# Optimization experiments

Hardware: AMD Instinct MI355X
Metric: run time of the kernel (lower is better)

The kernel has to match this reference:

```python
import jax, jax.numpy as jnp
import numpy as np
from functools import partial

NUM_CLUSTERS = 64
KMEANS_ITERS = 10  # fixed Lloyd iterations standing in for sklearn's converged fit


def _assign(points, centers):
    # points: [M, D], centers: [K, D] -> labels [M]
    # squared L2 distance via expansion; the -|x|^2 term is constant per point
    d = jnp.sum(centers * centers, axis=1)[None, :] - 2.0 * (points @ centers.T)
    return jnp.argmin(d, axis=1)


def _kmeans_fit_predict(points, num_clusters, iters):
    # Deterministic init: first K points (fixed-seed sklearn stand-in).
    centers0 = points[:num_clusters]

    def step(centers, _):
        labels = _assign(points, centers)
        sums = jax.ops.segment_sum(points, labels, num_segments=num_clusters)
        counts = jax.ops.segment_sum(jnp.ones((points.shape[0],), points.dtype),
                                     labels, num_segments=num_clusters)
        new_centers = jnp.where(counts[:, None] > 0, sums / jnp.maximum(counts, 1.0)[:, None], centers)
        return new_centers, None

    centers, _ = jax.lax.scan(step, centers0, None, length=iters)
    labels = _assign(points, centers)
    return labels, centers


def setup_inputs() -> dict:
    key = jax.random.key(0)
    k1, k2, k3 = jax.random.split(key, 3)
    B, N, D = 16, 4096, 384
    x = jax.random.normal(k1, (B, N, D), dtype=jnp.float32)
    # nn.Linear(feature_dim, feature_dim): weight [out, in], bias [out]
    scale = 1.0 / np.sqrt(D)
    W = jax.random.uniform(k2, (D, D), dtype=jnp.float32, minval=-scale, maxval=scale)
    b = jax.random.uniform(k3, (D,), dtype=jnp.float32, minval=-scale, maxval=scale)
    return {"x": x, "W": W, "b": b}


def reference(x, W, b):
    B, N, D = x.shape
    x_flat = jax.lax.stop_gradient(x.reshape(-1, D))  # torch does .detach() before kmeans
    labels, centers = _kmeans_fit_predict(x_flat, NUM_CLUSTERS, KMEANS_ITERS)
    clustered = centers[labels].reshape(B, N, D)
    return clustered @ W.T + b
```

## Files before the change

kernel.cpp:

```cpp
#include <hip/hip_runtime.h>

#define P_TOT 65536
#define DIM   384
#define KCL   64
#define ITERS 10
#define BPTS  256
#define NSB   8
#define BK    32
#define NKT   (DIM / BK)
#define LKA   36
#define LKB   68


__global__ __launch_bounds__(384) void init_kernel(const float* __restrict__ x,
                                                   float* __restrict__ centers,
                                                   float* __restrict__ cnorm,
                                                   float* __restrict__ cnt,
                                                   float* __restrict__ sums) {
    __shared__ float red[384];
    const int c = blockIdx.x, t = threadIdx.x;
    float v = x[(size_t)c * DIM + t];
    centers[(size_t)c * DIM + t] = v;
#pragma unroll
    for (int b = 0; b < NSB; ++b) sums[(size_t)b * KCL * DIM + (size_t)c * DIM + t] = 0.f;
    if (t == 0) cnt[c] = 0.f;
    red[t] = v * v;
    __syncthreads();
    if (t < 128) red[t] = red[t] + red[t + 128] + red[t + 256];
    __syncthreads();
    for (int s = 64; s > 0; s >>= 1) {
        if (t < s) red[t] += red[t + s];
        __syncthreads();
    }
    if (t == 0) cnorm[c] = red[0];
}

#define GEMM_ARGMIN_BODY(X, CENTERS, CNORM)                                          \
    const int t   = threadIdx.x;                                                     \
    const int cg  = t & 15;                               \
    const int pg  = t >> 4;                          \
    const int p0  = blockIdx.x * BPTS;                                               \
    const int spt = t >> 1;                             \
    const int sah = (t & 1) * 16;                      \
    const int sbc = t >> 3;                            \
    const int sbk = (t & 7) * 4;                \
    if (t < KCL) scn[t] = (CNORM)[t];                                                \
    float acc[8][4];                                                                 \
    _Pragma("unroll")                                                                \
    for (int i = 0; i < 8; ++i)                                                      \
        _Pragma("unroll")                                                            \
        for (int j = 0; j < 4; ++j) acc[i][j] = 0.f;                                 \
    const float* xrow = (X) + (size_t)(p0 + spt) * DIM;                              \
    const float* crow = (CENTERS) + (size_t)sbc * DIM;                               \
    float4 ra0 = *(const float4*)(xrow + sah);                                       \
    float4 ra1 = *(const float4*)(xrow + sah + 4);                                   \
    float4 ra2 = *(const float4*)(xrow + sah + 8);                                   \
    float4 ra3 = *(const float4*)(xrow + sah + 12);                                  \
    float4 rb  = *(const float4*)(crow + sbk);                                       \
    for (int kt = 0; kt < NKT; ++kt) {                                               \
        const int cur = kt & 1;                                                      \
        *(float4*)&At[cur][spt][sah + 0]  = ra0;                                     \
        *(float4*)&At[cur][spt][sah + 4]  = ra1;                                     \
        *(float4*)&At[cur][spt][sah + 8]  = ra2;                                     \
        *(float4*)&At[cur][spt][sah + 12] = ra3;                                     \
        Bt[cur][sbk + 0][sbc] = rb.x;  Bt[cur][sbk + 1][sbc] = rb.y;                 \
        Bt[cur][sbk + 2][sbc] = rb.z;  Bt[cur][sbk + 3][sbc] = rb.w;                 \
        if (kt + 1 < NKT) {                        \
            const int k0 = (kt + 1) * BK;                                            \
            ra0 = *(const float4*)(xrow + k0 + sah);                                 \
            ra1 = *(const float4*)(xrow + k0 + sah + 4);                             \
            ra2 = *(const float4*)(xrow + k0 + sah + 8);                             \
            ra3 = *(const float4*)(xrow + k0 + sah + 12);                            \
            rb  = *(const float4*)(crow + k0 + sbk);                                 \
        }                                                                            \
        __syncthreads();                  \
        _Pragma("unroll")                                                            \
        for (int kq = 0; kq < 8; ++kq) {                                             \
            float af[8][4];                                                          \
            _Pragma("unroll")                                                        \
            for (int i = 0; i < 8; ++i) {                                            \
                const float4 a4 = *(const float4*)&At[cur][pg * 8 + i][kq * 4];      \
                af[i][0] = a4.x; af[i][1] = a4.y; af[i][2] = a4.z; af[i][3] = a4.w;  \
            }                                                                        \
            _Pragma("unroll")                                                        \
            for (int kk = 0; kk < 4; ++kk) {                                         \
                const float4 bf = *(const float4*)&Bt[cur][kq * 4 + kk][cg * 4];     \
                _Pragma("unroll")                                                    \
                for (int i = 0; i < 8; ++i) {                                        \
                    acc[i][0] += af[i][kk] * bf.x;                                   \
                    acc[i][1] += af[i][kk] * bf.y;                                   \
                    acc[i][2] += af[i][kk] * bf.z;                                   \
                    acc[i][3] += af[i][kk] * bf.w;                                   \
                }                                                                    \
            }                                                                        \
        }                                                                            \
    }                                                                                \
    {                                                                                \
        float cn[4];                                                                 \
        _Pragma("unroll")                                                            \
        for (int j = 0; j < 4; ++j) cn[j] = scn[cg * 4 + j];                         \
        _Pragma("unroll")                                                            \
        for (int i = 0; i < 8; ++i) {                                                \
            float bvv = 3.4e38f; int bc = 0;                                         \
            _Pragma("unroll")                                                        \
            for (int j = 0; j < 4; ++j) {                                            \
                float d = cn[j] - 2.0f * acc[i][j];                                  \
                if (d < bvv) { bvv = d; bc = cg * 4 + j; }      \
            }                                                                        \
            _Pragma("unroll")                                                        \
            for (int m = 1; m < 16; m <<= 1) {       \
                const float ov = __shfl_xor(bvv, m, 64);                             \
                const int   oc = __shfl_xor(bc, m, 64);                              \
                if (ov < bvv || (ov == bvv && oc < bc)) { bvv = ov; bc = oc; }       \
            }                                                                        \
            if ((t & 15) == 0) lab[pg * 8 + i] = bc;                                 \
        }                                                                            \
    }                                                                                \
    __syncthreads();

__global__ __launch_bounds__(512, 2) void fused_kernel(const float* __restrict__ x,
                                                       const float* __restrict__ centers,
                                                       const float* __restrict__ cnorm,
                                                       float* __restrict__ sums,
                                                       float* __restrict__ cnt) {
    __shared__ float At[2][BPTS][LKA];
    __shared__ float Bt[2][BK][LKB];
    __shared__ float scn[KCL];
    __shared__ int   lab[BPTS];
    __shared__ int   lcnt[KCL];
    __shared__ int   lstart[KCL + 1];
    __shared__ int   lcur[KCL];
    __shared__ int   order[BPTS];

    if (threadIdx.x < KCL) lcnt[threadIdx.x] = 0;

    GEMM_ARGMIN_BODY(x, centers, cnorm)

    int myl = -1;
    if (t < BPTS) {
        myl = lab[t];
        atomicAdd(&lcnt[myl], 1);
    }
    __syncthreads();
    if (t < 64) {
        int v = lcnt[t];
        int s = v;
#pragma unroll
        for (int d = 1; d < 64; d <<= 1) {
            int u = __shfl_up(s, d, 64);
            if (t >= d) s += u;
        }
        lstart[t] = s - v;
        lcur[t] = s - v;
        if (t == 63) lstart[64] = s;
    }
    __syncthreads();
    if (t < BPTS) {
        int pos = atomicAdd(&lcur[myl], 1);
        order[pos] = t;
    }
    __syncthreads();

    if (t < DIM) {
        const float* xb = x + (size_t)p0 * DIM;
        float* sb = sums + (size_t)(blockIdx.x & (NSB - 1)) * KCL * DIM;
        int   curc = lab[order[0]];
        float run  = 0.f;
        for (int j0 = 0; j0 < BPTS; j0 += 8) {
            float v[8]; int cc[8];
#pragma unroll
            for (int u = 0; u < 8; ++u) {
                const int p = order[j0 + u];
                cc[u] = lab[p];
                v[u]  = xb[(size_t)p * DIM + t];
            }
#pragma unroll
            for (int u = 0; u < 8; ++u) {
                if (cc[u] != curc) {
                    atomicAdd(&sb[curc * DIM + t], run);
                    run = 0.f; curc = cc[u];
                }
                run += v[u];
            }
        }
        atomicAdd(&sb[curc * DIM + t], run);
    }
    if (t < KCL && lcnt[t] > 0) atomicAdd(&cnt[t], (float)lcnt[t]);
}

__global__ __launch_bounds__(512, 2) void label_kernel(const float* __restrict__ x,
                                                       const float* __restrict__ centers,
                                                       const float* __restrict__ cnorm,
                                                       int* __restrict__ labs) {
    __shared__ float At[2][BPTS][LKA];
    __shared__ float Bt[2][BK][LKB];
    __shared__ float scn[KCL];
    __shared__ int   lab[BPTS];

    GEMM_ARGMIN_BODY(x, centers, cnorm)

    if (t < BPTS) labs[p0 + t] = lab[t];
}

__global__ __launch_bounds__(384) void update_kernel(float* __restrict__ sums,
                                                     float* __restrict__ cnt,
                                                     float* __restrict__ centers,
                                                     float* __restrict__ cnorm) {
    __shared__ float red[384];
    const int c = blockIdx.x, t = threadIdx.x;
    float s = 0.f;
#pragma unroll
    for (int b = 0; b < NSB; ++b) {
        const size_t idx = (size_t)b * KCL * DIM + (size_t)c * DIM + t;
        s += sums[idx];
        sums[idx] = 0.f;
    }
    float n = cnt[c];
    float oldv = centers[(size_t)c * DIM + t];
    float nc = (n > 0.f) ? (s / n) : oldv;
    centers[(size_t)c * DIM + t] = nc;
    red[t] = nc * nc;
    __syncthreads();
    if (t == 0) cnt[c] = 0.f;
    if (t < 128) red[t] = red[t] + red[t + 128] + red[t + 256];
    __syncthreads();
    for (int st = 64; st > 0; st >>= 1) {
        if (t < st) red[t] += red[t + st];
        __syncthreads();
    }
    if (t == 0) cnorm[c] = red[0];
}

__global__ __launch_bounds__(384) void cw_kernel(const float* __restrict__ centers,
                                                 const float* __restrict__ W,
                                                 const float* __restrict__ b,
                                                 float* __restrict__ CW) {
    __shared__ float cs[DIM];
    const int c = blockIdx.x, j = threadIdx.x;
    cs[j] = centers[(size_t)c * DIM + j];
    __syncthreads();
    float acc = b[j];
    const float* wr = W + (size_t)j * DIM;
    for (int d4 = 0; d4 < 96; ++d4) {
        float4 v = *(const float4*)(wr + d4 * 4);
        acc += cs[d4 * 4 + 0] * v.x + cs[d4 * 4 + 1] * v.y
             + cs[d4 * 4 + 2] * v.z + cs[d4 * 4 + 3] * v.w;
    }
    CW[(size_t)c * DIM + j] = acc;
}

__global__ __launch_bounds__(256) void gather_kernel(const int* __restrict__ labs,
                                                     const float* __restrict__ CW,
                                                     float* __restrict__ out) {
    __shared__ int lab[32];
    const int t = threadIdx.x;
    const int p0 = blockIdx.x * 32;
    if (t < 32) lab[t] = labs[p0 + t];
    __syncthreads();
    const int pp = t >> 3;
    const int j0 = t & 7;
    const float* src = CW + (size_t)lab[pp] * DIM;
    float* dst = out + (size_t)(p0 + pp) * DIM;
#pragma unroll
    for (int r = 0; r < 12; ++r) {
        const int jg = (r * 8 + j0) * 4;
        *(float4*)(dst + jg) = *(const float4*)(src + jg);
    }
}

extern "C" void kernel_launch(void* const* d_in, const int* in_sizes, int n_in,
                              void* d_out, int out_size, void* d_ws, size_t ws_size,
                              hipStream_t stream) {
    const float* x = (const float*)d_in[0];
    const float* W = (const float*)d_in[1];
    const float* b = (const float*)d_in[2];
    float* out = (float*)d_out;

    float* centers = (float*)d_ws;
    float* cnorm   = centers + KCL * DIM;
    float* cnt     = cnorm + KCL;
    float* CW      = cnt + KCL;
    float* sums    = CW + KCL * DIM;
    int* labs      = (int*)sums;

    init_kernel<<<KCL, 384, 0, stream>>>(x, centers, cnorm, cnt, sums);
    for (int it = 0; it < ITERS; ++it) {
        fused_kernel<<<P_TOT / BPTS, 512, 0, stream>>>(x, centers, cnorm, sums, cnt);
        update_kernel<<<KCL, 384, 0, stream>>>(sums, cnt, centers, cnorm);
    }
    cw_kernel<<<KCL, 384, 0, stream>>>(centers, W, b, CW);
    label_kernel<<<P_TOT / BPTS, 512, 0, stream>>>(x, centers, cnorm, labs);
    gather_kernel<<<P_TOT / 32, 256, 0, stream>>>(labs, CW, out);
}
```

Before: 1.019 ms.

## Halve K-tile, raise occupancy to 4 blocks/CU, fuse label and gather kernels

Shrinks the shared-memory K tile from 32 to 16 so LDS per block drops, and raises the launch-bounds minimum blocks per CU from 2 to 4. The inner product loop is restructured so the B fragments are loaded once per k-quad instead of keeping an 8x4 A fragment array in registers. The final label and gather kernels are merged, so the output rows are written directly from CW using the shared-memory labels, removing one launch and the round trip of labels through global memory. The risks are more barriers per K step from the smaller tile and register spills under the tighter launch bound.

```diff
diff --git a/kernel.cpp b/kernel.cpp
--- a/kernel.cpp
+++ b/kernel.cpp
@@ -6,9 +6,9 @@
 #define ITERS 10
 #define BPTS  256
 #define NSB   8
-#define BK    32
+#define BK    16
 #define NKT   (DIM / BK)
-#define LKA   36
+#define LKA   20
 #define LKB   68
 
 
@@ -41,9 +41,9 @@
     const int pg  = t >> 4;                          \
     const int p0  = blockIdx.x * BPTS;                                               \
     const int spt = t >> 1;                             \
-    const int sah = (t & 1) * 16;                      \
+    const int sah = (t & 1) * 8;                        \
     const int sbc = t >> 3;                            \
-    const int sbk = (t & 7) * 4;                \
+    const int sbk = (t & 7) * 2;                \
     if (t < KCL) scn[t] = (CNORM)[t];                                                \
     float acc[8][4];                                                                 \
     _Pragma("unroll")                                                                \
@@ -54,44 +54,36 @@
     const float* crow = (CENTERS) + (size_t)sbc * DIM;                               \
     float4 ra0 = *(const float4*)(xrow + sah);                                       \
     float4 ra1 = *(const float4*)(xrow + sah + 4);                                   \
-    float4 ra2 = *(const float4*)(xrow + sah + 8);                                   \
-    float4 ra3 = *(const float4*)(xrow + sah + 12);                                  \
-    float4 rb  = *(const float4*)(crow + sbk);                                       \
+    float2 rb  = *(const float2*)(crow + sbk);                                       \
     for (int kt = 0; kt < NKT; ++kt) {                                               \
         const int cur = kt & 1;                                                      \
-        *(float4*)&At[cur][spt][sah + 0]  = ra0;                                     \
-        *(float4*)&At[cur][spt][sah + 4]  = ra1;                                     \
-        *(float4*)&At[cur][spt][sah + 8]  = ra2;                                     \
-        *(float4*)&At[cur][spt][sah + 12] = ra3;                                     \
+        *(float4*)&At[cur][spt][sah + 0] = ra0;                                      \
+        *(float4*)&At[cur][spt][sah + 4] = ra1;                                      \
         Bt[cur][sbk + 0][sbc] = rb.x;  Bt[cur][sbk + 1][sbc] = rb.y;                 \
-        Bt[cur][sbk + 2][sbc] = rb.z;  Bt[cur][sbk + 3][sbc] = rb.w;                 \
         if (kt + 1 < NKT) {                        \
             const int k0 = (kt + 1) * BK;                                            \
             ra0 = *(const float4*)(xrow + k0 + sah);                                 \
             ra1 = *(const float4*)(xrow + k0 + sah + 4);                             \
-            ra2 = *(const float4*)(xrow + k0 + sah + 8);                             \
-            ra3 = *(const float4*)(xrow + k0 + sah + 12);                            \
-            rb  = *(const float4*)(crow + k0 + sbk);                                 \
+            rb  = *(const float2*)(crow + k0 + sbk);                                 \
         }                                                                            \
         __syncthreads();                  \
         _Pragma("unroll")                                                            \
-        for (int kq = 0; kq < 8; ++kq) {                                             \
-            float af[8][4];                                                          \
+        for (int kq = 0; kq < 4; ++kq) {                                             \
+            const float4 bf0 = *(const float4*)&Bt[cur][kq * 4 + 0][cg * 4];         \
+            const float4 bf1 = *(const float4*)&Bt[cur][kq * 4 + 1][cg * 4];         \
+            const float4 bf2 = *(const float4*)&Bt[cur][kq * 4 + 2][cg * 4];         \
+            const float4 bf3 = *(const float4*)&Bt[cur][kq * 4 + 3][cg * 4];         \
             _Pragma("unroll")                                                        \
             for (int i = 0; i < 8; ++i) {                                            \
                 const float4 a4 = *(const float4*)&At[cur][pg * 8 + i][kq * 4];      \
-                af[i][0] = a4.x; af[i][1] = a4.y; af[i][2] = a4.z; af[i][3] = a4.w;  \
-            }                                                                        \
-            _Pragma("unroll")                                                        \
-            for (int kk = 0; kk < 4; ++kk) {                                         \
-                const float4 bf = *(const float4*)&Bt[cur][kq * 4 + kk][cg * 4];     \
-                _Pragma("unroll")                                                    \
-                for (int i = 0; i < 8; ++i) {                                        \
-                    acc[i][0] += af[i][kk] * bf.x;                                   \
-                    acc[i][1] += af[i][kk] * bf.y;                                   \
-                    acc[i][2] += af[i][kk] * bf.z;                                   \
-                    acc[i][3] += af[i][kk] * bf.w;                                   \
-                }                                                                    \
+                acc[i][0] += a4.x * bf0.x; acc[i][1] += a4.x * bf0.y;                \
+                acc[i][2] += a4.x * bf0.z; acc[i][3] += a4.x * bf0.w;                \
+                acc[i][0] += a4.y * bf1.x; acc[i][1] += a4.y * bf1.y;                \
+                acc[i][2] += a4.y * bf1.z; acc[i][3] += a4.y * bf1.w;                \
+                acc[i][0] += a4.z * bf2.x; acc[i][1] += a4.z * bf2.y;                \
+                acc[i][2] += a4.z * bf2.z; acc[i][3] += a4.z * bf2.w;                \
+                acc[i][0] += a4.w * bf3.x; acc[i][1] += a4.w * bf3.y;                \
+                acc[i][2] += a4.w * bf3.z; acc[i][3] += a4.w * bf3.w;                \
             }                                                                        \
         }                                                                            \
     }                                                                                \
@@ -118,7 +110,7 @@
     }                                                                                \
     __syncthreads();
 
-__global__ __launch_bounds__(512, 2) void fused_kernel(const float* __restrict__ x,
+__global__ __launch_bounds__(512, 4) void fused_kernel(const float* __restrict__ x,
                                                        const float* __restrict__ centers,
                                                        const float* __restrict__ cnorm,
                                                        float* __restrict__ sums,
@@ -188,10 +180,11 @@
     if (t < KCL && lcnt[t] > 0) atomicAdd(&cnt[t], (float)lcnt[t]);
 }
 
-__global__ __launch_bounds__(512, 2) void label_kernel(const float* __restrict__ x,
-                                                       const float* __restrict__ centers,
-                                                       const float* __restrict__ cnorm,
-                                                       int* __restrict__ labs) {
+__global__ __launch_bounds__(512, 4) void labelgather_kernel(const float* __restrict__ x,
+                                                             const float* __restrict__ centers,
+                                                             const float* __restrict__ cnorm,
+                                                             const float* __restrict__ CW,
+                                                             float* __restrict__ out) {
     __shared__ float At[2][BPTS][LKA];
     __shared__ float Bt[2][BK][LKB];
     __shared__ float scn[KCL];
@@ -199,7 +192,15 @@
 
     GEMM_ARGMIN_BODY(x, centers, cnorm)
 
-    if (t < BPTS) labs[p0 + t] = lab[t];
+    const float4* CW4 = (const float4*)CW;
+    float4* out4 = (float4*)(out + (size_t)p0 * DIM);
+#pragma unroll 4
+    for (int r = 0; r < 48; ++r) {
+        const int q  = r * 512 + t;
+        const int pp = q / 96;
+        const int jg = q - pp * 96;
+        out4[(size_t)pp * 96 + jg] = CW4[(size_t)lab[pp] * 96 + jg];
+    }
 }
 
 __global__ __launch_bounds__(384) void update_kernel(float* __restrict__ sums,
@@ -249,25 +250,6 @@
     CW[(size_t)c * DIM + j] = acc;
 }
 
-__global__ __launch_bounds__(256) void gather_kernel(const int* __restrict__ labs,
-                                                     const float* __restrict__ CW,
-                                                     float* __restrict__ out) {
-    __shared__ int lab[32];
-    const int t = threadIdx.x;
-    const int p0 = blockIdx.x * 32;
-    if (t < 32) lab[t] = labs[p0 + t];
-    __syncthreads();
-    const int pp = t >> 3;
-    const int j0 = t & 7;
-    const float* src = CW + (size_t)lab[pp] * DIM;
-    float* dst = out + (size_t)(p0 + pp) * DIM;
-#pragma unroll
-    for (int r = 0; r < 12; ++r) {
-        const int jg = (r * 8 + j0) * 4;
-        *(float4*)(dst + jg) = *(const float4*)(src + jg);
-    }
-}
-
 extern "C" void kernel_launch(void* const* d_in, const int* in_sizes, int n_in,
                               void* d_out, int out_size, void* d_ws, size_t ws_size,
                               hipStream_t stream) {
@@ -281,7 +263,6 @@
     float* cnt     = cnorm + KCL;
     float* CW      = cnt + KCL;
     float* sums    = CW + KCL * DIM;
-    int* labs      = (int*)sums;
 
     init_kernel<<<KCL, 384, 0, stream>>>(x, centers, cnorm, cnt, sums);
     for (int it = 0; it < ITERS; ++it) {
@@ -289,6 +270,5 @@
         update_kernel<<<KCL, 384, 0, stream>>>(sums, cnt, centers, cnorm);
     }
     cw_kernel<<<KCL, 384, 0, stream>>>(centers, W, b, CW);
-    label_kernel<<<P_TOT / BPTS, 512, 0, stream>>>(x, centers, cnorm, labs);
-    gather_kernel<<<P_TOT / 32, 256, 0, stream>>>(labs, CW, out);
-}
+    labelgather_kernel<<<P_TOT / BPTS, 512, 0, stream>>>(x, centers, cnorm, CW, out);
+}
```

Measured after the change: 1.256 ms. 23.2% more time.
